# Kernel tuning notes

Measured on AMD Instinct MI355X. Metric: run time of the kernel, lower is better.

Reference implementation:

```python
import jax, jax.numpy as jnp
import numpy as np

N_NODES = 10000
N_EDGES = 160000
D_IN = 512
D_HID = 1024

def setup_inputs() -> dict:
    key = jax.random.key(0)
    ks = jax.random.split(key, 8)
    feat = jax.random.normal(ks[0], (N_NODES, D_IN), dtype=jnp.float32)
    W1 = jax.random.normal(ks[1], (D_IN, D_HID), dtype=jnp.float32) * (1.0 / np.sqrt(D_IN))
    b1 = jnp.zeros((D_HID,), dtype=jnp.float32)
    W2 = jax.random.normal(ks[2], (D_HID, D_IN), dtype=jnp.float32) * (1.0 / np.sqrt(D_HID))
    b2 = jnp.zeros((D_IN,), dtype=jnp.float32)
    eps = jnp.zeros((1,), dtype=jnp.float32)
    src = jax.random.randint(ks[3], (N_EDGES,), 0, N_NODES, dtype=jnp.int32)
    dst = jax.random.randint(ks[4], (N_EDGES,), 0, N_NODES, dtype=jnp.int32)
    return {"feat": feat, "W1": W1, "b1": b1, "W2": W2, "b2": b2,
            "eps": eps, "src": src, "dst": dst}

def reference(feat, W1, b1, W2, b2, eps, src, dst):
    # message passing: copy src feature along each edge, sum-reduce at dst
    msgs = feat[src]                                   # [E, D_IN] gather
    neigh = jax.ops.segment_sum(msgs, dst, num_segments=feat.shape[0])  # [N, D_IN]
    # GIN combine: (1 + eps) * self + sum(neighbors)
    rst = (1.0 + eps[0]) * feat + neigh
    # apply_func: 2-layer MLP with ReLU
    h = jnp.maximum(rst @ W1 + b1, 0.0)
    h = h @ W2 + b2
    # identity residual (in_dim == out_dim)
    return h + feat
```

## Files before the change

kernel.cpp:

```cpp
#include <hip/hip_runtime.h>

typedef unsigned short u16;
typedef unsigned int u32;
typedef __bf16 bf16x8 __attribute__((ext_vector_type(8)));
typedef float f32x4 __attribute__((ext_vector_type(4)));

#define N_NODES 10000
#define N_EDGES 160000
#define D_IN 512
#define D_HID 1024

#define AS1 __attribute__((address_space(1)))
#define AS3 __attribute__((address_space(3)))

__device__ __forceinline__ u16 f2bf(float f) {
    union { float f; u32 u; } v; v.f = f;
    return (u16)((v.u + 0x7fffu + ((v.u >> 16) & 1u)) >> 16);
}
__device__ __forceinline__ float b2f(u32 h) {
    union { u32 u; float f; } v; v.u = h << 16; return v.f;
}

__global__ void hist_k(const int* __restrict__ dst, int* __restrict__ counts) {
    int e = blockIdx.x * 256 + threadIdx.x;
    if (e < N_EDGES) atomicAdd(&counts[dst[e]], 1);
}

__global__ __launch_bounds__(1024) void scan_k(const int* __restrict__ counts,
                                               int* __restrict__ offs,
                                               int* __restrict__ cursor) {
    __shared__ int wpre[16];
    int t = threadIdx.x, l = t & 63, w = t >> 6;
    int base = t * 10;
    int c[10];
    int lsum = 0;
#pragma unroll
    for (int i = 0; i < 10; i++) {
        int idx = base + i;
        c[i] = (idx < N_NODES) ? counts[idx] : 0;
        lsum += c[i];
    }
    int sc = lsum;
#pragma unroll
    for (int d = 1; d < 64; d <<= 1) {
        int v = __shfl_up(sc, d);
        if (l >= d) sc += v;
    }
    __shared__ int wsum[16];
    if (l == 63) wsum[w] = sc;
    __syncthreads();
    if (w == 0 && l < 16) {
        int v = wsum[l];
        int p = v;
#pragma unroll
        for (int d = 1; d < 16; d <<= 1) {
            int u = __shfl_up(p, d);
            if (l >= d) p += u;
        }
        wpre[l] = p - v;
    }
    __syncthreads();
    int run = wpre[w] + sc - lsum;
#pragma unroll
    for (int i = 0; i < 10; i++) {
        int idx = base + i;
        if (idx < N_NODES) { offs[idx] = run; cursor[idx] = run; run += c[i]; }
    }
    if (t == 1023) offs[N_NODES] = wpre[15] + sc;
}

__global__ void reorder_k(const int* __restrict__ src, const int* __restrict__ dst,
                          int* __restrict__ cursor, int* __restrict__ ssrc) {
    int e = blockIdx.x * 256 + threadIdx.x;
    if (e >= N_EDGES) return;
    int d = dst[e];
    int pos = atomicAdd(&cursor[d], 1);
    ssrc[pos] = src[e];
}

__global__ void cvt_bf16_k(const float* __restrict__ in, u16* __restrict__ out, int n) {
    int i = (blockIdx.x * 256 + threadIdx.x) * 8;
    if (i >= n) return;
    float4 a = *(const float4*)(in + i);
    float4 b = *(const float4*)(in + i + 4);
    uint4 o;
    o.x = (u32)f2bf(a.x) | ((u32)f2bf(a.y) << 16);
    o.y = (u32)f2bf(a.z) | ((u32)f2bf(a.w) << 16);
    o.z = (u32)f2bf(b.x) | ((u32)f2bf(b.y) << 16);
    o.w = (u32)f2bf(b.z) | ((u32)f2bf(b.w) << 16);
    *(uint4*)(out + i) = o;
}

__global__ void transw_k(const float* __restrict__ W1, u16* __restrict__ w1t,
                         const float* __restrict__ W2, u16* __restrict__ w2t) {
    __shared__ float tile[32][33];
    int b = blockIdx.x;
    const float* W; u16* WT; int K, N, nt;
    if (b < 512) { W = W1; WT = w1t; K = D_IN;  N = D_HID; nt = 32; }
    else         { b -= 512; W = W2; WT = w2t; K = D_HID; N = D_IN;  nt = 16; }
    int n0 = (b % nt) * 32, k0 = (b / nt) * 32;
    int tx = threadIdx.x, ty = threadIdx.y;
#pragma unroll
    for (int i = 0; i < 32; i += 8)
        tile[ty + i][tx] = W[(size_t)(k0 + ty + i) * N + n0 + tx];
    __syncthreads();
#pragma unroll
    for (int i = 0; i < 32; i += 8)
        WT[(size_t)(n0 + ty + i) * K + k0 + tx] = f2bf(tile[tx][ty + i]);
}

__global__ __launch_bounds__(128) void gather_k(const float* __restrict__ feat,
                                                const u16* __restrict__ featb,
                                                const float* __restrict__ eps,
                                                const int* __restrict__ offs,
                                                const int* __restrict__ ssrc,
                                                u16* __restrict__ out) {
    int n = (blockIdx.x * 128 + threadIdx.x) >> 6;
    int l = threadIdx.x & 63;
    if (n >= N_NODES) return;
    int beg = offs[n], end = offs[n + 1];
    float s = 1.0f + eps[0];
    float4 s0 = *(const float4*)(feat + (size_t)n * D_IN + l * 8);
    float4 s1 = *(const float4*)(feat + (size_t)n * D_IN + l * 8 + 4);
    float acc[8] = { s * s0.x, s * s0.y, s * s0.z, s * s0.w,
                     s * s1.x, s * s1.y, s * s1.z, s * s1.w };
    int e = beg;
    for (; e + 4 <= end; e += 4) {
        int i0 = ssrc[e], i1 = ssrc[e + 1], i2 = ssrc[e + 2], i3 = ssrc[e + 3];
        uint4 v0 = *(const uint4*)(featb + (size_t)i0 * D_IN + l * 8);
        uint4 v1 = *(const uint4*)(featb + (size_t)i1 * D_IN + l * 8);
        uint4 v2 = *(const uint4*)(featb + (size_t)i2 * D_IN + l * 8);
        uint4 v3 = *(const uint4*)(featb + (size_t)i3 * D_IN + l * 8);
#define ACC4(v) \
        acc[0] += b2f(v.x & 0xffffu); acc[1] += b2f(v.x >> 16); \
        acc[2] += b2f(v.y & 0xffffu); acc[3] += b2f(v.y >> 16); \
        acc[4] += b2f(v.z & 0xffffu); acc[5] += b2f(v.z >> 16); \
        acc[6] += b2f(v.w & 0xffffu); acc[7] += b2f(v.w >> 16);
        ACC4(v0) ACC4(v1) ACC4(v2) ACC4(v3)
    }
    for (; e < end; e++) {
        int i0 = ssrc[e];
        uint4 v0 = *(const uint4*)(featb + (size_t)i0 * D_IN + l * 8);
        ACC4(v0)
    }
#undef ACC4
    uint4 o;
    o.x = (u32)f2bf(acc[0]) | ((u32)f2bf(acc[1]) << 16);
    o.y = (u32)f2bf(acc[2]) | ((u32)f2bf(acc[3]) << 16);
    o.z = (u32)f2bf(acc[4]) | ((u32)f2bf(acc[5]) << 16);
    o.w = (u32)f2bf(acc[6]) | ((u32)f2bf(acc[7]) << 16);
    *(uint4*)(out + (size_t)n * D_IN + l * 8) = o;
}

template <int EPI>
__global__ __launch_bounds__(256) void gemm_k(const u16* __restrict__ A,
                                              const u16* __restrict__ BT,
                                              const float* __restrict__ bias,
                                              const float* __restrict__ feat,
                                              void* __restrict__ Cout,
                                              int M, int N, int K) {
    __shared__ __bf16 sA[2][128 * 64];
    __shared__ __bf16 sB[2][128 * 64];
    const int row0 = blockIdx.y * 128;
    const int col0 = blockIdx.x * 128;
    const int t = threadIdx.x;
    const int w = t >> 6, l = t & 63;
    const int wm = (w >> 1) * 64, wn = (w & 1) * 64;
    const int lr = l & 15;
    const int lq = l >> 4;

    const u16* pA[4];
    const u16* pB[4];
    int loff[4];
    {
        int rloc = w * 32 + (l >> 3);
        int gch8 = (((l & 7) ^ (l >> 3)) * 8);
#pragma unroll
        for (int q = 0; q < 4; q++) {
            int ar = row0 + rloc + q * 8; if (ar > M - 1) ar = M - 1;
            pA[q] = A + (size_t)ar * K + gch8;
            int br = col0 + rloc + q * 8;
            pB[q] = BT + (size_t)br * K + gch8;
            loff[q] = (w * 32 + q * 8) * 64;
        }
    }
    const int fo = ((lq ^ (lr & 7)) * 8);

    f32x4 acc[4][4] = {};

    auto STAGE = [&](int buf, int kk0) {
#pragma unroll
        for (int q = 0; q < 4; q++) {
            __builtin_amdgcn_global_load_lds((const AS1 void*)(pA[q] + kk0),
                                             (AS3 void*)(&sA[buf][loff[q]]), 16, 0, 0);
            __builtin_amdgcn_global_load_lds((const AS1 void*)(pB[q] + kk0),
                                             (AS3 void*)(&sB[buf][loff[q]]), 16, 0, 0);
        }
    };

    STAGE(0, 0);
    int cur = 0;
    for (int k0 = 0; k0 < K; k0 += 64, cur ^= 1) {
        int kn = (k0 + 64 < K) ? (k0 + 64) : k0;
        STAGE(cur ^ 1, kn);
        asm volatile("s_waitcnt vmcnt(8)" ::: "memory");
        __builtin_amdgcn_s_barrier();
#pragma unroll
        for (int kk = 0; kk < 64; kk += 32) {
            const int fx = fo ^ kk;
            bf16x8 fa[4], fb[4];
#pragma unroll
            for (int i = 0; i < 4; i++)
                fa[i] = *(const bf16x8*)(&sA[cur][0] + (wm + i * 16 + lr) * 64 + fx);
#pragma unroll
            for (int j = 0; j < 4; j++)
                fb[j] = *(const bf16x8*)(&sB[cur][0] + (wn + j * 16 + lr) * 64 + fx);
#pragma unroll
            for (int i = 0; i < 4; i++)
#pragma unroll
                for (int j = 0; j < 4; j++)
                    acc[i][j] = __builtin_amdgcn_mfma_f32_16x16x32_bf16(
                        fa[i], fb[j], acc[i][j], 0, 0, 0);
        }
        __builtin_amdgcn_s_barrier();
    }

#pragma unroll
    for (int i = 0; i < 4; i++) {
        int rowb = row0 + wm + i * 16 + lq * 4;
#pragma unroll
        for (int j = 0; j < 4; j++) {
            int col = col0 + wn + j * 16 + lr;
            float bv = bias[col];
#pragma unroll
            for (int r = 0; r < 4; r++) {
                int rr = rowb + r;
                if (rr < M) {
                    float v = acc[i][j][r] + bv;
                    if (EPI == 0) {
                        v = fmaxf(v, 0.0f);
                        ((u16*)Cout)[(size_t)rr * N + col] = f2bf(v);
                    } else {
                        v += feat[(size_t)rr * N + col];
                        ((float*)Cout)[(size_t)rr * N + col] = v;
                    }
                }
            }
        }
    }
}

extern "C" void kernel_launch(void* const* d_in, const int* in_sizes, int n_in,
                              void* d_out, int out_size, void* d_ws, size_t ws_size,
                              hipStream_t stream) {
    const float* feat = (const float*)d_in[0];
    const float* W1   = (const float*)d_in[1];
    const float* b1   = (const float*)d_in[2];
    const float* W2   = (const float*)d_in[3];
    const float* b2   = (const float*)d_in[4];
    const float* eps  = (const float*)d_in[5];
    const int*   src  = (const int*)d_in[6];
    const int*   dst  = (const int*)d_in[7];
    float* out = (float*)d_out;

    char* ws = (char*)d_ws;
    u16* rst_b16 = (u16*)(ws);
    u16* h_b16   = (u16*)(ws + 10240000);
    u16* featb   = (u16*)(ws + 30720000);
    u16* w1t     = (u16*)(ws + 40960000);
    u16* w2t     = (u16*)(ws + 42008576);
    int* counts  = (int*)(ws + 43057152);
    int* offs    = (int*)(ws + 43097152);
    int* cursor  = (int*)(ws + 43137160);
    int* ssrc    = (int*)(ws + 43177160);

    const int NE = N_NODES * D_IN;

    hipMemsetAsync(counts, 0, N_NODES * sizeof(int), stream);
    hist_k<<<(N_EDGES + 255) / 256, 256, 0, stream>>>(dst, counts);
    scan_k<<<1, 1024, 0, stream>>>(counts, offs, cursor);
    reorder_k<<<(N_EDGES + 255) / 256, 256, 0, stream>>>(src, dst, cursor, ssrc);

    cvt_bf16_k<<<NE / 8 / 256, 256, 0, stream>>>(feat, featb, NE);
    transw_k<<<1024, dim3(32, 8), 0, stream>>>(W1, w1t, W2, w2t);

    gather_k<<<(N_NODES + 1) / 2, 128, 0, stream>>>(feat, featb, eps, offs, ssrc, rst_b16);

    const int MT = (N_NODES + 127) / 128;
    gemm_k<0><<<dim3(D_HID / 128, MT), 256, 0, stream>>>(rst_b16, w1t, b1, nullptr,
                                                         (void*)h_b16, N_NODES, D_HID, D_IN);
    gemm_k<1><<<dim3(D_IN / 128, MT), 256, 0, stream>>>(h_b16, w2t, b2, feat,
                                                        (void*)out, N_NODES, D_IN, D_HID);
}
```

Before: 221.8 us.

## Use 4-stage BK=32 LDS pipeline with XCD-aware tile remapping in GEMM

```diff
diff --git a/kernel.cpp b/kernel.cpp
--- a/kernel.cpp
+++ b/kernel.cpp
@@ -153,76 +153,87 @@
 }
 
 template <int EPI>
-__global__ __launch_bounds__(256) void gemm_k(const u16* __restrict__ A,
-                                              const u16* __restrict__ BT,
-                                              const float* __restrict__ bias,
-                                              const float* __restrict__ feat,
-                                              void* __restrict__ Cout,
-                                              int M, int N, int K) {
-    __shared__ __bf16 sA[2][128 * 64];
-    __shared__ __bf16 sB[2][128 * 64];
-    const int row0 = blockIdx.y * 128;
-    const int col0 = blockIdx.x * 128;
+__global__ __launch_bounds__(256, 2) void gemm_k(const u16* __restrict__ A,
+                                                 const u16* __restrict__ BT,
+                                                 const float* __restrict__ bias,
+                                                 const float* __restrict__ feat,
+                                                 void* __restrict__ Cout,
+                                                 int M, int N, int K) {
+    __shared__ __bf16 sA[4][128 * 32];
+    __shared__ __bf16 sB[4][128 * 32];
+
+    const int NX = gridDim.x;
+    const int nwg = NX * gridDim.y;
+    const int flat = blockIdx.y * NX + blockIdx.x;
+    const int qq = nwg >> 3, rr8 = nwg & 7;
+    const int xcd = flat & 7, idx = flat >> 3;
+    const int L = (xcd < rr8 ? xcd * (qq + 1) : rr8 * (qq + 1) + (xcd - rr8) * qq) + idx;
+    const int row0 = (L / NX) * 128;
+    const int col0 = (L % NX) * 128;
+
     const int t = threadIdx.x;
     const int w = t >> 6, l = t & 63;
     const int wm = (w >> 1) * 64, wn = (w & 1) * 64;
     const int lr = l & 15;
     const int lq = l >> 4;
 
-    const u16* pA[4];
-    const u16* pB[4];
-    int loff[4];
+    const u16* pA[2];
+    const u16* pB[2];
+    int ldo[2];
     {
-        int rloc = w * 32 + (l >> 3);
-        int gch8 = (((l & 7) ^ (l >> 3)) * 8);
-#pragma unroll
-        for (int q = 0; q < 4; q++) {
-            int ar = row0 + rloc + q * 8; if (ar > M - 1) ar = M - 1;
-            pA[q] = A + (size_t)ar * K + gch8;
-            int br = col0 + rloc + q * 8;
-            pB[q] = BT + (size_t)br * K + gch8;
-            loff[q] = (w * 32 + q * 8) * 64;
+        int g8 = (((l & 3) ^ ((l >> 3) & 3)) * 8);
+        int rl = l >> 2;
+#pragma unroll
+        for (int h = 0; h < 2; h++) {
+            int R = w * 32 + h * 16;
+            int ar = row0 + R + rl; if (ar > M - 1) ar = M - 1;
+            pA[h] = A + (size_t)ar * K + g8;
+            int br = col0 + R + rl;
+            pB[h] = BT + (size_t)br * K + g8;
+            ldo[h] = R * 32;
         }
     }
-    const int fo = ((lq ^ (lr & 7)) * 8);
+    const int fo = ((lq ^ ((lr >> 1) & 3)) * 8);
 
     f32x4 acc[4][4] = {};
-
-    auto STAGE = [&](int buf, int kk0) {
-#pragma unroll
-        for (int q = 0; q < 4; q++) {
-            __builtin_amdgcn_global_load_lds((const AS1 void*)(pA[q] + kk0),
-                                             (AS3 void*)(&sA[buf][loff[q]]), 16, 0, 0);
-            __builtin_amdgcn_global_load_lds((const AS1 void*)(pB[q] + kk0),
-                                             (AS3 void*)(&sB[buf][loff[q]]), 16, 0, 0);
+    const int NT = K >> 5;
+
+    auto STAGE = [&](int buf, int kt) {
+        const int ko = kt << 5;
+#pragma unroll
+        for (int h = 0; h < 2; h++) {
+            __builtin_amdgcn_global_load_lds((const AS1 void*)(pA[h] + ko),
+                                             (AS3 void*)(&sA[buf][ldo[h]]), 16, 0, 0);
+            __builtin_amdgcn_global_load_lds((const AS1 void*)(pB[h] + ko),
+                                             (AS3 void*)(&sB[buf][ldo[h]]), 16, 0, 0);
         }
     };
 
     STAGE(0, 0);
-    int cur = 0;
-    for (int k0 = 0; k0 < K; k0 += 64, cur ^= 1) {
-        int kn = (k0 + 64 < K) ? (k0 + 64) : k0;
-        STAGE(cur ^ 1, kn);
+    STAGE(1, 1);
+    STAGE(2, 2);
+
+    for (int it = 0; it < NT; ++it) {
         asm volatile("s_waitcnt vmcnt(8)" ::: "memory");
+        __builtin_amdgcn_sched_barrier(0);
         __builtin_amdgcn_s_barrier();
-#pragma unroll
-        for (int kk = 0; kk < 64; kk += 32) {
-            const int fx = fo ^ kk;
-            bf16x8 fa[4], fb[4];
-#pragma unroll
-            for (int i = 0; i < 4; i++)
-                fa[i] = *(const bf16x8*)(&sA[cur][0] + (wm + i * 16 + lr) * 64 + fx);
+        int kt = it + 3;
+        STAGE((it + 3) & 3, kt < NT ? kt : 0);
+        const __bf16* cA = &sA[it & 3][0];
+        const __bf16* cB = &sB[it & 3][0];
+        bf16x8 fa[4], fb[4];
+#pragma unroll
+        for (int i = 0; i < 4; i++)
+            fa[i] = *(const bf16x8*)(cA + (wm + i * 16 + lr) * 32 + fo);
+#pragma unroll
+        for (int j = 0; j < 4; j++)
+            fb[j] = *(const bf16x8*)(cB + (wn + j * 16 + lr) * 32 + fo);
+#pragma unroll
+        for (int i = 0; i < 4; i++)
 #pragma unroll
             for (int j = 0; j < 4; j++)
-                fb[j] = *(const bf16x8*)(&sB[cur][0] + (wn + j * 16 + lr) * 64 + fx);
-#pragma unroll
-            for (int i = 0; i < 4; i++)
-#pragma unroll
-                for (int j = 0; j < 4; j++)
-                    acc[i][j] = __builtin_amdgcn_mfma_f32_16x16x32_bf16(
-                        fa[i], fb[j], acc[i][j], 0, 0, 0);
-        }
-        __builtin_amdgcn_s_barrier();
+                acc[i][j] = __builtin_amdgcn_mfma_f32_16x16x32_bf16(
+                    fa[i], fb[j], acc[i][j], 0, 0, 0);
     }
 
 #pragma unroll
```

Measured after the change: 228.9 us. 3.2% more time.
